# Kernel tuning notes

Measured on AMD Instinct MI355X. Metric: run time of the kernel, lower is better.

Reference implementation:

```python
import jax, jax.numpy as jnp
import numpy as np


def setup_inputs() -> dict:
    key = jax.random.key(0)
    k1, k2 = jax.random.split(key)
    B, C, N = 8, 11, 64  # batch, fragment channels, cubic voxel grid edge
    inp = jax.random.normal(k1, (B, C, N, N, N), dtype=jnp.float32)
    tar = jax.random.normal(k2, (B, C, N, N, N), dtype=jnp.float32)
    # 20 contiguous bins spanning [-4, 4]; bin_range[k] = (lo_k, hi_k)
    edges = jnp.linspace(-4.0, 4.0, 21, dtype=jnp.float32)
    bin_range = jnp.stack([edges[:-1], edges[1:]], axis=-1)  # [20, 2]
    return {"inp": inp, "tar": tar, "bin_range": bin_range}


def _bin_data(x, bin_range):
    # x: [B, C, nx, ny, nz] -> normalized histogram [B, C, K]
    B, C = x.shape[0], x.shape[1]
    nvox = x.shape[2] * x.shape[3] * x.shape[4]
    xf = x.reshape(B, C, -1)  # [B, C, nvox]

    def count_one_bin(b):  # b: [2] = (lo, hi)
        return jnp.sum((xf >= b[0]) & (xf < b[1]), axis=-1).astype(jnp.float32)

    # sequential over K bins (small, fixed) to avoid a [K,B,C,nvox] mask blowup
    counts = jax.lax.map(count_one_bin, bin_range)  # [K, B, C]
    return jnp.transpose(counts, (1, 2, 0)) / jnp.float32(nvox)


def _smooth_l1(a, b):
    # torch.nn.SmoothL1Loss default: beta=1.0, mean reduction
    d = jnp.abs(a - b)
    return jnp.mean(jnp.where(d < 1.0, 0.5 * d * d, d - 0.5))


def reference(inp, tar, bin_range):
    loss1 = _smooth_l1(inp, tar)
    loss2 = jnp.mean(jnp.abs(_bin_data(inp, bin_range) - _bin_data(tar, bin_range)))
    return 0.5 * loss1 + 0.5 * loss2
```

## Files before the change

kernel.cpp:

```cpp
#include <hip/hip_runtime.h>

#define BC 88
#define NVOX 262144
#define KBINS 20
#define THREADS 256
#define NBLOCKS 2048
#define CHUNK 1024
#define CPB 11
#define CPC 256
#define HSTRIDE 23
#define NSUB 64

__global__ void __launch_bounds__(THREADS, 8)
binloss_main(const float* __restrict__ inp, const float* __restrict__ tar,
             const float* __restrict__ br, int* __restrict__ g_hist,
             float* __restrict__ partials)
{
    __shared__ int   rows[NSUB * HSTRIDE];
    __shared__ float wsum[THREADS / 64];

    const int tid = threadIdx.x;
    for (int i = tid; i < NSUB * HSTRIDE; i += THREADS) rows[i] = 0;

    const float e0     = br[0];
    const float eK     = br[2 * KBINS - 1];
    const float inv_w  = (float)KBINS / (eK - e0);
    const float shift1 = 1.0f - e0 * inv_w;
    const float tmax   = (float)(KBINS + 1) + 0.5f;
    __syncthreads();

    const int fc  = blockIdx.x * CPB;
    const int ch0 = fc >> 8;
    const int rem = fc & (CPC - 1);
    const int n1  = (rem + CPB > CPC) ? (CPC - rem) : CPB;

    const float4* ip4 = (const float4*)inp;
    const float4* tp4 = (const float4*)tar;
    int* myrow = &rows[(tid & 63) * HSTRIDE];

    float s_lin = 0.f, s_quad = 0.f;

#pragma unroll 2
    for (int c = fc; c < fc + n1; ++c) {
        float4 a = ip4[(size_t)c * 256 + tid];
        float4 b = tp4[(size_t)c * 256 + tid];
#pragma unroll
        for (int q = 0; q < 4; ++q) {
            float av = (&a.x)[q], bv = (&b.x)[q];
            float d = fabsf(av - bv);
            s_lin += fmaxf(d, 1.0f);
            float m = fminf(d, 1.0f);
            s_quad  = __builtin_fmaf(m, m, s_quad);
            int sa = (int)__builtin_amdgcn_fmed3f(__builtin_fmaf(av, inv_w, shift1), 0.0f, tmax);
            int sb = (int)__builtin_amdgcn_fmed3f(__builtin_fmaf(bv, inv_w, shift1), 0.0f, tmax);
            atomicAdd(&myrow[sa], 1);
            atomicAdd(&myrow[sb], -1);
        }
    }
    __syncthreads();
    if (tid < 80) {
        int bin = tid % KBINS, qr = tid / KBINS;
        int s = 0;
#pragma unroll
        for (int r = qr * 16; r < qr * 16 + 16; ++r) s += rows[r * HSTRIDE + 1 + bin];
        atomicAdd(&g_hist[ch0 * KBINS + bin], s);
    }

    if (n1 < CPB) {
        __syncthreads();
        for (int i = tid; i < NSUB * HSTRIDE; i += THREADS) rows[i] = 0;
        __syncthreads();
#pragma unroll 2
        for (int c = fc + n1; c < fc + CPB; ++c) {
            float4 a = ip4[(size_t)c * 256 + tid];
            float4 b = tp4[(size_t)c * 256 + tid];
#pragma unroll
            for (int q = 0; q < 4; ++q) {
                float av = (&a.x)[q], bv = (&b.x)[q];
                float d = fabsf(av - bv);
                s_lin += fmaxf(d, 1.0f);
                float m = fminf(d, 1.0f);
                s_quad  = __builtin_fmaf(m, m, s_quad);
                int sa = (int)__builtin_amdgcn_fmed3f(__builtin_fmaf(av, inv_w, shift1), 0.0f, tmax);
                int sb = (int)__builtin_amdgcn_fmed3f(__builtin_fmaf(bv, inv_w, shift1), 0.0f, tmax);
                atomicAdd(&myrow[sa], 1);
                atomicAdd(&myrow[sb], -1);
            }
        }
        __syncthreads();
        if (tid < 80) {
            int bin = tid % KBINS, qr = tid / KBINS;
            int s = 0;
#pragma unroll
            for (int r = qr * 16; r < qr * 16 + 16; ++r) s += rows[r * HSTRIDE + 1 + bin];
            atomicAdd(&g_hist[(ch0 + 1) * KBINS + bin], s);
        }
    }

    float sl1 = (s_lin - (float)(CPB * 4)) + 0.5f * s_quad;
#pragma unroll
    for (int off = 32; off > 0; off >>= 1) sl1 += __shfl_down(sl1, off, 64);
    if ((tid & 63) == 0) wsum[tid >> 6] = sl1;
    __syncthreads();
    if (tid == 0)
        partials[blockIdx.x] = wsum[0] + wsum[1] + wsum[2] + wsum[3];
}

__global__ void __launch_bounds__(256)
binloss_final(const int* __restrict__ g_hist, const float* __restrict__ partials,
              float* __restrict__ out)
{
    __shared__ double r1[256];
    __shared__ double r2[256];
    const int tid = threadIdx.x;
    double s1 = 0.0, s2 = 0.0;
    for (int i = tid; i < NBLOCKS; i += 256) s1 += (double)partials[i];
    for (int i = tid; i < BC * KBINS; i += 256) s2 += fabs((double)g_hist[i]);
    r1[tid] = s1; r2[tid] = s2;
    __syncthreads();
    for (int off = 128; off > 0; off >>= 1) {
        if (tid < off) { r1[tid] += r1[tid + off]; r2[tid] += r2[tid + off]; }
        __syncthreads();
    }
    if (tid == 0) {
        const double ntot  = (double)BC * (double)NVOX;
        double loss1 = r1[0] / ntot;
        double loss2 = r2[0] / ((double)NVOX * (double)(BC * KBINS));
        out[0] = (float)(0.5 * loss1 + 0.5 * loss2);
    }
}

extern "C" void kernel_launch(void* const* d_in, const int* in_sizes, int n_in,
                              void* d_out, int out_size, void* d_ws, size_t ws_size,
                              hipStream_t stream) {
    const float* inp = (const float*)d_in[0];
    const float* tar = (const float*)d_in[1];
    const float* br  = (const float*)d_in[2];

    int*   g_hist   = (int*)d_ws;
    float* partials = (float*)((char*)d_ws + BC * KBINS * sizeof(int));

    hipMemsetAsync(d_ws, 0, BC * KBINS * sizeof(int), stream);

    binloss_main<<<NBLOCKS, THREADS, 0, stream>>>(inp, tar, br, g_hist, partials);
    binloss_final<<<1, 256, 0, stream>>>(g_hist, partials, (float*)d_out);
}
```

Baseline: 44.73 us.

## Fully unroll per-block loads and use dual LDS histograms to remove channel-split path

Replaces the loop over 11 chunks with all global loads issued up front in two batches, so more memory requests are in flight per thread. A second LDS histogram set replaces the separate boundary-crossing pass and its extra barriers and clears, with each chunk picking its histogram by index. The final flush handles both sets in one step and skips zero adds. In exchange the kernel uses more registers and twice the LDS, and launch bounds drop to 4 blocks per SIMD, which may lower occupancy.

```diff
diff --git a/kernel.cpp b/kernel.cpp
--- a/kernel.cpp
+++ b/kernel.cpp
@@ -5,28 +5,28 @@
 #define KBINS 20
 #define THREADS 256
 #define NBLOCKS 2048
-#define CHUNK 1024
 #define CPB 11
 #define CPC 256
 #define HSTRIDE 23
 #define NSUB 64
+#define ROWSET (NSUB * HSTRIDE)
 
-__global__ void __launch_bounds__(THREADS, 8)
+__global__ void __launch_bounds__(THREADS, 4)
 binloss_main(const float* __restrict__ inp, const float* __restrict__ tar,
              const float* __restrict__ br, int* __restrict__ g_hist,
              float* __restrict__ partials)
 {
-    __shared__ int   rows[NSUB * HSTRIDE];
+    __shared__ int   rows[2 * ROWSET];
     __shared__ float wsum[THREADS / 64];
 
     const int tid = threadIdx.x;
-    for (int i = tid; i < NSUB * HSTRIDE; i += THREADS) rows[i] = 0;
+    for (int i = tid; i < 2 * ROWSET; i += THREADS) rows[i] = 0;
 
     const float e0     = br[0];
     const float eK     = br[2 * KBINS - 1];
     const float inv_w  = (float)KBINS / (eK - e0);
     const float shift1 = 1.0f - e0 * inv_w;
-    const float tmax   = (float)(KBINS + 1) + 0.5f;
+    const float tmax   = 21.5f;
     __syncthreads();
 
     const int fc  = blockIdx.x * CPB;
@@ -34,16 +34,15 @@
     const int rem = fc & (CPC - 1);
     const int n1  = (rem + CPB > CPC) ? (CPC - rem) : CPB;
 
-    const float4* ip4 = (const float4*)inp;
-    const float4* tp4 = (const float4*)tar;
-    int* myrow = &rows[(tid & 63) * HSTRIDE];
+    const float4* pa = (const float4*)inp + (size_t)fc * 256 + tid;
+    const float4* pb = (const float4*)tar + (size_t)fc * 256 + tid;
+
+    int* r0 = &rows[(tid & 63) * HSTRIDE];
+    int* r1 = r0 + ROWSET;
 
     float s_lin = 0.f, s_quad = 0.f;
 
-#pragma unroll 2
-    for (int c = fc; c < fc + n1; ++c) {
-        float4 a = ip4[(size_t)c * 256 + tid];
-        float4 b = tp4[(size_t)c * 256 + tid];
+    auto proc = [&](float4 a, float4 b, int* rw) {
 #pragma unroll
         for (int q = 0; q < 4; ++q) {
             float av = (&a.x)[q], bv = (&b.x)[q];
@@ -53,57 +52,53 @@
             s_quad  = __builtin_fmaf(m, m, s_quad);
             int sa = (int)__builtin_amdgcn_fmed3f(__builtin_fmaf(av, inv_w, shift1), 0.0f, tmax);
             int sb = (int)__builtin_amdgcn_fmed3f(__builtin_fmaf(bv, inv_w, shift1), 0.0f, tmax);
-            atomicAdd(&myrow[sa], 1);
-            atomicAdd(&myrow[sb], -1);
+            atomicAdd(&rw[sa], 1);
+            atomicAdd(&rw[sb], -1);
         }
-    }
-    __syncthreads();
-    if (tid < 80) {
-        int bin = tid % KBINS, qr = tid / KBINS;
-        int s = 0;
-#pragma unroll
-        for (int r = qr * 16; r < qr * 16 + 16; ++r) s += rows[r * HSTRIDE + 1 + bin];
-        atomicAdd(&g_hist[ch0 * KBINS + bin], s);
-    }
+    };
 
-    if (n1 < CPB) {
-        __syncthreads();
-        for (int i = tid; i < NSUB * HSTRIDE; i += THREADS) rows[i] = 0;
-        __syncthreads();
-#pragma unroll 2
-        for (int c = fc + n1; c < fc + CPB; ++c) {
-            float4 a = ip4[(size_t)c * 256 + tid];
-            float4 b = tp4[(size_t)c * 256 + tid];
-#pragma unroll
-            for (int q = 0; q < 4; ++q) {
-                float av = (&a.x)[q], bv = (&b.x)[q];
-                float d = fabsf(av - bv);
-                s_lin += fmaxf(d, 1.0f);
-                float m = fminf(d, 1.0f);
-                s_quad  = __builtin_fmaf(m, m, s_quad);
-                int sa = (int)__builtin_amdgcn_fmed3f(__builtin_fmaf(av, inv_w, shift1), 0.0f, tmax);
-                int sb = (int)__builtin_amdgcn_fmed3f(__builtin_fmaf(bv, inv_w, shift1), 0.0f, tmax);
-                atomicAdd(&myrow[sa], 1);
-                atomicAdd(&myrow[sb], -1);
-            }
-        }
-        __syncthreads();
-        if (tid < 80) {
-            int bin = tid % KBINS, qr = tid / KBINS;
-            int s = 0;
-#pragma unroll
-            for (int r = qr * 16; r < qr * 16 + 16; ++r) s += rows[r * HSTRIDE + 1 + bin];
-            atomicAdd(&g_hist[(ch0 + 1) * KBINS + bin], s);
-        }
-    }
+    float4 A0 = pa[0 * 256], A1 = pa[1 * 256], A2 = pa[2 * 256], A3 = pa[3 * 256];
+    float4 B0 = pb[0 * 256], B1 = pb[1 * 256], B2 = pb[2 * 256], B3 = pb[3 * 256];
+    float4 C0 = pa[4 * 256], C1 = pa[5 * 256], C2 = pa[6 * 256], C3 = pa[7 * 256];
+    float4 D0 = pb[4 * 256], D1 = pb[5 * 256], D2 = pb[6 * 256], D3 = pb[7 * 256];
+
+    proc(A0, B0, (0 < n1) ? r0 : r1);
+    proc(A1, B1, (1 < n1) ? r0 : r1);
+    proc(A2, B2, (2 < n1) ? r0 : r1);
+    proc(A3, B3, (3 < n1) ? r0 : r1);
+
+    float4 E0 = pa[8 * 256], E1 = pa[9 * 256], E2 = pa[10 * 256];
+    float4 F0 = pb[8 * 256], F1 = pb[9 * 256], F2 = pb[10 * 256];
+
+    proc(C0, D0, (4 < n1) ? r0 : r1);
+    proc(C1, D1, (5 < n1) ? r0 : r1);
+    proc(C2, D2, (6 < n1) ? r0 : r1);
+    proc(C3, D3, (7 < n1) ? r0 : r1);
+    proc(E0, F0, (8 < n1) ? r0 : r1);
+    proc(E1, F1, (9 < n1) ? r0 : r1);
+    proc(E2, F2, (10 < n1) ? r0 : r1);
 
     float sl1 = (s_lin - (float)(CPB * 4)) + 0.5f * s_quad;
 #pragma unroll
     for (int off = 32; off > 0; off >>= 1) sl1 += __shfl_down(sl1, off, 64);
     if ((tid & 63) == 0) wsum[tid >> 6] = sl1;
     __syncthreads();
+
     if (tid == 0)
         partials[blockIdx.x] = wsum[0] + wsum[1] + wsum[2] + wsum[3];
+
+    if (tid < 160) {
+        const int set = tid / 80, t2 = tid % 80;
+        const int bin = t2 % KBINS, qr = t2 / KBINS;
+        const int ch  = ch0 + set;
+        if (ch < BC) {
+            int s = 0;
+#pragma unroll
+            for (int r = qr * 16; r < qr * 16 + 16; ++r)
+                s += rows[set * ROWSET + r * HSTRIDE + 1 + bin];
+            if (s) atomicAdd(&g_hist[ch * KBINS + bin], s);
+        }
+    }
 }
 
 __global__ void __launch_bounds__(256)
```

Result: no change. 44.07 us, median of 2 (-1.5%).

## Bin target values into per-thread packed byte-counter registers instead of LDS atomics

Applied to the files above, without the earlier changes.

Input values still go to the shared-memory atomic histogram, but target values now build a per-thread cumulative histogram of 21 edge bytes packed into three 64-bit registers, with branchless adds. The packed counters are written to shared memory at the end and reduced per edge, and the bin counts come from differences of adjacent cumulative counts. This halves the LDS atomic traffic at the cost of extra ALU work, a larger shared footprint (brow) and a more complex reduction. The two-channel split is folded into one loop that flushes partial histograms at the boundary, and the occupancy hint in launch_bounds is dropped.

```diff
diff --git a/kernel.cpp b/kernel.cpp
--- a/kernel.cpp
+++ b/kernel.cpp
@@ -3,30 +3,33 @@
 #define BC 88
 #define NVOX 262144
 #define KBINS 20
+#define NEDGE 21
 #define THREADS 256
 #define NBLOCKS 2048
-#define CHUNK 1024
 #define CPB 11
 #define CPC 256
 #define HSTRIDE 23
-#define NSUB 64
+#define ROWSET (64 * HSTRIDE)
 
-__global__ void __launch_bounds__(THREADS, 8)
+__global__ void __launch_bounds__(THREADS)
 binloss_main(const float* __restrict__ inp, const float* __restrict__ tar,
              const float* __restrict__ br, int* __restrict__ g_hist,
              float* __restrict__ partials)
 {
-    __shared__ int   rows[NSUB * HSTRIDE];
-    __shared__ float wsum[THREADS / 64];
+    __shared__ int          rows[ROWSET];
+    __shared__ unsigned int brow[THREADS][7];
+    __shared__ int          aq[4][KBINS],  bq[4][NEDGE];
+    __shared__ int          aq0[4][KBINS], bq0[4][NEDGE];
+    __shared__ float        wsum[4];
 
-    const int tid = threadIdx.x;
-    for (int i = tid; i < NSUB * HSTRIDE; i += THREADS) rows[i] = 0;
+    const int tid = threadIdx.x, lane = tid & 63;
+    for (int i = tid; i < ROWSET; i += THREADS) rows[i] = 0;
 
     const float e0     = br[0];
     const float eK     = br[2 * KBINS - 1];
     const float inv_w  = (float)KBINS / (eK - e0);
     const float shift1 = 1.0f - e0 * inv_w;
-    const float tmax   = (float)(KBINS + 1) + 0.5f;
+    const float tmax   = 21.5f;
     __syncthreads();
 
     const int fc  = blockIdx.x * CPB;
@@ -34,16 +37,45 @@
     const int rem = fc & (CPC - 1);
     const int n1  = (rem + CPB > CPC) ? (CPC - rem) : CPB;
 
-    const float4* ip4 = (const float4*)inp;
-    const float4* tp4 = (const float4*)tar;
-    int* myrow = &rows[(tid & 63) * HSTRIDE];
+    const float4* pa = (const float4*)inp + (size_t)fc * 256 + tid;
+    const float4* pb = (const float4*)tar + (size_t)fc * 256 + tid;
 
+    int* rw = &rows[lane * HSTRIDE];
+
+    const unsigned long long ONES  = 0x0101010101010101ull;
+    const unsigned long long BIASC = 0x8080808080808080ull;
+    unsigned long long H0 = BIASC, H1 = BIASC, H2 = BIASC;
     float s_lin = 0.f, s_quad = 0.f;
 
-#pragma unroll 2
-    for (int c = fc; c < fc + n1; ++c) {
-        float4 a = ip4[(size_t)c * 256 + tid];
-        float4 b = tp4[(size_t)c * 256 + tid];
+    for (int k = 0; k < CPB; ++k) {
+        if (k == n1) {
+            __syncthreads();
+            brow[tid][0] = (unsigned int)H0; brow[tid][1] = (unsigned int)(H0 >> 32);
+            brow[tid][2] = (unsigned int)H1; brow[tid][3] = (unsigned int)(H1 >> 32);
+            brow[tid][4] = (unsigned int)H2; brow[tid][5] = (unsigned int)(H2 >> 32);
+            H0 = BIASC; H1 = BIASC; H2 = BIASC;
+            __syncthreads();
+            if (tid < 80) {
+                const int j = tid % KBINS, qr = tid / KBINS;
+                int s = 0;
+#pragma unroll
+                for (int rr = qr * 16; rr < qr * 16 + 16; ++rr)
+                    s += rows[rr * HSTRIDE + 1 + j];
+                aq0[qr][j] = s;
+            } else if (tid < 164) {
+                const int idx = tid - 80, qr = idx / NEDGE, j = idx % NEDGE;
+                const int dw = j >> 2, sh = 8 * (j & 3);
+                int s = 0;
+                for (int r = qr * 64; r < qr * 64 + 64; ++r)
+                    s += (int)((brow[r][dw] >> sh) & 0xFFu);
+                bq0[qr][j] = s;
+            }
+            __syncthreads();
+            for (int i = tid; i < ROWSET; i += THREADS) rows[i] = 0;
+            __syncthreads();
+        }
+        float4 a = pa[k * 256];
+        float4 b = pb[k * 256];
 #pragma unroll
         for (int q = 0; q < 4; ++q) {
             float av = (&a.x)[q], bv = (&b.x)[q];
@@ -52,58 +84,62 @@
             float m = fminf(d, 1.0f);
             s_quad  = __builtin_fmaf(m, m, s_quad);
             int sa = (int)__builtin_amdgcn_fmed3f(__builtin_fmaf(av, inv_w, shift1), 0.0f, tmax);
+            atomicAdd(&rw[sa], 1);
             int sb = (int)__builtin_amdgcn_fmed3f(__builtin_fmaf(bv, inv_w, shift1), 0.0f, tmax);
-            atomicAdd(&myrow[sa], 1);
-            atomicAdd(&myrow[sb], -1);
-        }
-    }
-    __syncthreads();
-    if (tid < 80) {
-        int bin = tid % KBINS, qr = tid / KBINS;
-        int s = 0;
-#pragma unroll
-        for (int r = qr * 16; r < qr * 16 + 16; ++r) s += rows[r * HSTRIDE + 1 + bin];
-        atomicAdd(&g_hist[ch0 * KBINS + bin], s);
-    }
-
-    if (n1 < CPB) {
-        __syncthreads();
-        for (int i = tid; i < NSUB * HSTRIDE; i += THREADS) rows[i] = 0;
-        __syncthreads();
-#pragma unroll 2
-        for (int c = fc + n1; c < fc + CPB; ++c) {
-            float4 a = ip4[(size_t)c * 256 + tid];
-            float4 b = tp4[(size_t)c * 256 + tid];
-#pragma unroll
-            for (int q = 0; q < 4; ++q) {
-                float av = (&a.x)[q], bv = (&b.x)[q];
-                float d = fabsf(av - bv);
-                s_lin += fmaxf(d, 1.0f);
-                float m = fminf(d, 1.0f);
-                s_quad  = __builtin_fmaf(m, m, s_quad);
-                int sa = (int)__builtin_amdgcn_fmed3f(__builtin_fmaf(av, inv_w, shift1), 0.0f, tmax);
-                int sb = (int)__builtin_amdgcn_fmed3f(__builtin_fmaf(bv, inv_w, shift1), 0.0f, tmax);
-                atomicAdd(&myrow[sa], 1);
-                atomicAdd(&myrow[sb], -1);
-            }
-        }
-        __syncthreads();
-        if (tid < 80) {
-            int bin = tid % KBINS, qr = tid / KBINS;
-            int s = 0;
-#pragma unroll
-            for (int r = qr * 16; r < qr * 16 + 16; ++r) s += rows[r * HSTRIDE + 1 + bin];
-            atomicAdd(&g_hist[(ch0 + 1) * KBINS + bin], s);
+            unsigned long long P = ONES << ((8 * sb) & 63);
+            bool l8 = sb < 8, l16 = sb < 16;
+            H0 += l8 ? P : 0ull;
+            H1 += l8 ? ONES : (l16 ? P : 0ull);
+            H2 += l16 ? ONES : P;
         }
     }
 
     float sl1 = (s_lin - (float)(CPB * 4)) + 0.5f * s_quad;
 #pragma unroll
     for (int off = 32; off > 0; off >>= 1) sl1 += __shfl_down(sl1, off, 64);
-    if ((tid & 63) == 0) wsum[tid >> 6] = sl1;
+    if (lane == 0) wsum[tid >> 6] = sl1;
+
+    brow[tid][0] = (unsigned int)H0; brow[tid][1] = (unsigned int)(H0 >> 32);
+    brow[tid][2] = (unsigned int)H1; brow[tid][3] = (unsigned int)(H1 >> 32);
+    brow[tid][4] = (unsigned int)H2; brow[tid][5] = (unsigned int)(H2 >> 32);
     __syncthreads();
+
     if (tid == 0)
         partials[blockIdx.x] = wsum[0] + wsum[1] + wsum[2] + wsum[3];
+
+    if (tid < 80) {
+        const int j = tid % KBINS, qr = tid / KBINS;
+        int s = 0;
+#pragma unroll
+        for (int rr = qr * 16; rr < qr * 16 + 16; ++rr)
+            s += rows[rr * HSTRIDE + 1 + j];
+        aq[qr][j] = s;
+    } else if (tid < 164) {
+        const int idx = tid - 80, qr = idx / NEDGE, j = idx % NEDGE;
+        const int dw = j >> 2, sh = 8 * (j & 3);
+        int s = 0;
+        for (int r = qr * 64; r < qr * 64 + 64; ++r)
+            s += (int)((brow[r][dw] >> sh) & 0xFFu);
+        bq[qr][j] = s;
+    }
+    __syncthreads();
+
+    const int ch_last = (n1 < CPB) ? ch0 + 1 : ch0;
+    if (tid < KBINS) {
+        const int j = tid;
+        int a4  = aq[0][j] + aq[1][j] + aq[2][j] + aq[3][j];
+        int blo = bq[0][j] + bq[1][j] + bq[2][j] + bq[3][j];
+        int bhi = bq[0][j + 1] + bq[1][j + 1] + bq[2][j + 1] + bq[3][j + 1];
+        int v = a4 - (bhi - blo);
+        if (v) atomicAdd(&g_hist[ch_last * KBINS + j], v);
+    } else if (tid >= 64 && tid < 64 + KBINS && n1 < CPB) {
+        const int j = tid - 64;
+        int a4  = aq0[0][j] + aq0[1][j] + aq0[2][j] + aq0[3][j];
+        int blo = bq0[0][j] + bq0[1][j] + bq0[2][j] + bq0[3][j];
+        int bhi = bq0[0][j + 1] + bq0[1][j + 1] + bq0[2][j + 1] + bq0[3][j + 1];
+        int v = a4 - (bhi - blo);
+        if (v) atomicAdd(&g_hist[ch0 * KBINS + j], v);
+    }
 }
 
 __global__ void __launch_bounds__(256)
```

Result: slower. 46.15 us (+3.2%).
